# Kernel tuning notes

Measured on AMD Instinct MI355X. Metric: run time of the kernel, lower is better.

The kernel has to match this reference:

```python
import jax, jax.numpy as jnp
import numpy as np

TOPK = 2
ROUTED_SCALING_FACTOR = 1.0


def setup_inputs() -> dict:
    key = jax.random.key(0)
    k1, k2 = jax.random.split(key)
    N, D, E = 8192, 4096, 64
    x = jax.random.normal(k1, (N, D), dtype=jnp.float32)
    expert_embeddings = jax.random.normal(k2, (E, D), dtype=jnp.float32) * 0.02
    gate_bias = jnp.zeros((E,), dtype=jnp.float32)
    return {"x": x, "expert_embeddings": expert_embeddings, "gate_bias": gate_bias}


def reference(x, expert_embeddings, gate_bias):
    # logits: (N, E) = x @ W^T, computed in fp32 as in the original
    logits = jnp.einsum('nd,ed->ne', x.astype(jnp.float32), expert_embeddings.astype(jnp.float32))
    scores = jax.nn.sigmoid(logits)
    biased_scores = scores + gate_bias  # bias only affects expert selection
    _, indices = jax.lax.top_k(biased_scores, TOPK)  # (N, topk)
    weights = jnp.take_along_axis(scores, indices, axis=-1)  # gather unbiased scores
    weights = weights / jnp.sum(weights, axis=-1, keepdims=True)
    weights = weights * ROUTED_SCALING_FACTOR
    return weights, indices, scores
```

## Files before the change

### kernel.cpp

```cpp
#include <hip/hip_runtime.h>
#include <hip/hip_bf16.h>
#include <math.h>

#define NROWS 8192
#define DDIM  4096
#define NEXP  64
#define KSPLIT 16
#define KCHUNK (DDIM / KSPLIT)
#define KSTEPS (KCHUNK / 32)

typedef __attribute__((ext_vector_type(8))) short bf16x8;
typedef __attribute__((ext_vector_type(4))) float f32x4;

__device__ inline unsigned short bf16_rne(float f) {
    unsigned u = __builtin_bit_cast(unsigned, f);
    u += 0x7FFF + ((u >> 16) & 1);
    return (unsigned short)(u >> 16);
}

__device__ inline void split8(const float* xf, bf16x8& hi, bf16x8& lo) {
#pragma unroll
    for (int j = 0; j < 8; j++) {
        const unsigned short h = bf16_rne(xf[j]);
        const float hf = __builtin_bit_cast(float, (unsigned)h << 16);
        hi[j] = (short)h;
        lo[j] = (short)bf16_rne(xf[j] - hf);
    }
}

__global__ __launch_bounds__(256) void wfrag_kernel(
    const float* __restrict__ w, unsigned short* __restrict__ whi,
    unsigned short* __restrict__ wlo, float* __restrict__ logits)
{
    const int kc = blockIdx.x;
    const int t  = threadIdx.x >> 6;
    const int l  = threadIdx.x & 63;
    const int e  = t * 16 + (l & 15);
    const int k0 = kc * 32 + ((l >> 4) * 8);
    const float* p = w + (size_t)e * DDIM + k0;
    float xf[8];
    *(float4*)&xf[0] = *(const float4*)p;
    *(float4*)&xf[4] = *(const float4*)(p + 4);
    bf16x8 hi, lo;
    split8(xf, hi, lo);
    const size_t off = ((size_t)(kc * 4 + t) * 64 + l) * 8;
    *(bf16x8*)(whi + off) = hi;
    *(bf16x8*)(wlo + off) = lo;

    const float4 z = {0.f, 0.f, 0.f, 0.f};
    float4* lz = (float4*)logits;
    const int base = (blockIdx.x * 256 + threadIdx.x) * 4;
#pragma unroll
    for (int j = 0; j < 4; j++) lz[base + j] = z;
}

__global__ __launch_bounds__(256) void gemm_partial_kernel(
    const float* __restrict__ x, const unsigned short* __restrict__ whi,
    const unsigned short* __restrict__ wlo, float* __restrict__ logits)
{
    const int tid = threadIdx.x;
    const int wv  = tid >> 6;
    const int l   = tid & 63;
    const int q   = l >> 4;
    const int col = l & 15;
    const int r0  = blockIdx.x * 128 + wv * 32;
    const int kh  = blockIdx.y;
    const int kb  = kh * KCHUNK;

    const float* xp0 = x + (size_t)(r0 + col) * DDIM + kb + q * 8;
    const float* xp1 = xp0 + (size_t)16 * DDIM;
    const unsigned short* bhp = whi + ((size_t)(kb / 32) * 4 * 64 + l) * 8;
    const unsigned short* blp = wlo + ((size_t)(kb / 32) * 4 * 64 + l) * 8;

    f32x4 acc[2][4];
#pragma unroll
    for (int m = 0; m < 2; m++)
#pragma unroll
        for (int t = 0; t < 4; t++) acc[m][t] = f32x4{0, 0, 0, 0};

    float xf[2][2][8];
    *(float4*)&xf[0][0][0] = *(const float4*)(xp0);
    *(float4*)&xf[0][0][4] = *(const float4*)(xp0 + 4);
    *(float4*)&xf[0][1][0] = *(const float4*)(xp1);
    *(float4*)&xf[0][1][4] = *(const float4*)(xp1 + 4);

    for (int s = 0; s < KSTEPS; s++) {
        const int cur = s & 1, nxt = cur ^ 1;

        bf16x8 bh[4], bl[4];
        const unsigned short* bhs = bhp + (size_t)s * 4 * 64 * 8;
        const unsigned short* bls = blp + (size_t)s * 4 * 64 * 8;
#pragma unroll
        for (int t = 0; t < 4; t++) {
            bh[t] = *(const bf16x8*)(bhs + (size_t)t * 64 * 8);
            bl[t] = *(const bf16x8*)(bls + (size_t)t * 64 * 8);
        }

        if (s + 1 < KSTEPS) {
            const float* xn0 = xp0 + (s + 1) * 32;
            const float* xn1 = xp1 + (s + 1) * 32;
            *(float4*)&xf[nxt][0][0] = *(const float4*)(xn0);
            *(float4*)&xf[nxt][0][4] = *(const float4*)(xn0 + 4);
            *(float4*)&xf[nxt][1][0] = *(const float4*)(xn1);
            *(float4*)&xf[nxt][1][4] = *(const float4*)(xn1 + 4);
        }

        bf16x8 ah[2], al[2];
        split8(xf[cur][0], ah[0], al[0]);
        split8(xf[cur][1], ah[1], al[1]);
#pragma unroll
        for (int m = 0; m < 2; m++)
#pragma unroll
            for (int t = 0; t < 4; t++) {
                acc[m][t] = __builtin_amdgcn_mfma_f32_16x16x32_bf16(ah[m], bh[t], acc[m][t], 0, 0, 0);
                acc[m][t] = __builtin_amdgcn_mfma_f32_16x16x32_bf16(ah[m], bl[t], acc[m][t], 0, 0, 0);
                acc[m][t] = __builtin_amdgcn_mfma_f32_16x16x32_bf16(al[m], bh[t], acc[m][t], 0, 0, 0);
            }
    }

#pragma unroll
    for (int m = 0; m < 2; m++)
#pragma unroll
        for (int t = 0; t < 4; t++)
#pragma unroll
            for (int r = 0; r < 4; r++)
                unsafeAtomicAdd(
                    &logits[(size_t)(r0 + m * 16 + q * 4 + r) * NEXP + t * 16 + col],
                    acc[m][t][r]);
}

__global__ __launch_bounds__(256) void gate_topk_kernel(
    const float* __restrict__ logits, const float* __restrict__ bias,
    float* __restrict__ out)
{
    const int tid = threadIdx.x;
    const int e   = tid & 63;
    const int row = blockIdx.x * 4 + (tid >> 6);
    const size_t idx = (size_t)row * NEXP + e;

    const float logit = logits[idx];
    const float score = 1.0f / (1.0f + expf(-logit));
    out[(size_t)4 * NROWS + idx] = score;

    const float biased = score + bias[e];

    float v = biased; int bi = e;
#pragma unroll
    for (int off = 32; off; off >>= 1) {
        const float ov = __shfl_xor(v, off);
        const int   oi = __shfl_xor(bi, off);
        if (ov > v || (ov == v && oi < bi)) { v = ov; bi = oi; }
    }
    const int i1 = bi;

    float v2 = (e == i1) ? -INFINITY : biased;
    int bi2 = e;
#pragma unroll
    for (int off = 32; off; off >>= 1) {
        const float ov = __shfl_xor(v2, off);
        const int   oi = __shfl_xor(bi2, off);
        if (ov > v2 || (ov == v2 && oi < bi2)) { v2 = ov; bi2 = oi; }
    }
    const int i2 = bi2;

    const float s1 = __shfl(score, i1);
    const float s2 = __shfl(score, i2);
    if (e == 0) {
        const float inv = 1.0f / (s1 + s2);
        out[(size_t)row * 2 + 0] = s1 * inv;
        out[(size_t)row * 2 + 1] = s2 * inv;
        out[(size_t)2 * NROWS + row * 2 + 0] = (float)i1;
        out[(size_t)2 * NROWS + row * 2 + 1] = (float)i2;
    }
}

extern "C" void kernel_launch(void* const* d_in, const int* in_sizes, int n_in,
                              void* d_out, int out_size, void* d_ws, size_t ws_size,
                              hipStream_t stream)
{
    const float* x    = (const float*)d_in[0];
    const float* w    = (const float*)d_in[1];
    const float* bias = (const float*)d_in[2];
    float* out  = (float*)d_out;

    float* logits = (float*)d_ws;
    const size_t logits_bytes = (size_t)NROWS * NEXP * 4;
    unsigned short* whi = (unsigned short*)((char*)d_ws + logits_bytes);
    unsigned short* wlo = whi + (size_t)NEXP * DDIM;

    wfrag_kernel<<<DDIM / 32, 256, 0, stream>>>(w, whi, wlo, logits);
    dim3 g1(NROWS / 128, KSPLIT);
    gemm_partial_kernel<<<g1, 256, 0, stream>>>(x, whi, wlo, logits);
    gate_topk_kernel<<<NROWS / 4, 256, 0, stream>>>(logits, bias, out);
}
```

Baseline: 214.6 us.

## Fuse gate/top-k into split-K GEMM via last-block counter

Removes the separate gate_topk kernel. Each row-tile keeps an atomic counter, and the last of the KSPLIT blocks to finish runs the sigmoid, top-2 and normalization for its 128 rows. This saves one kernel launch and a global re-read pass over the logits, but the epilogue is serialized onto a few late blocks and the kernel gains extra fences and atomics.

```diff
diff --git a/kernel.cpp b/kernel.cpp
--- a/kernel.cpp
+++ b/kernel.cpp
@@ -30,7 +30,8 @@
 
 __global__ __launch_bounds__(256) void wfrag_kernel(
     const float* __restrict__ w, unsigned short* __restrict__ whi,
-    unsigned short* __restrict__ wlo, float* __restrict__ logits)
+    unsigned short* __restrict__ wlo, float* __restrict__ logits,
+    unsigned* __restrict__ cnt)
 {
     const int kc = blockIdx.x;
     const int t  = threadIdx.x >> 6;
@@ -52,12 +53,18 @@
     const int base = (blockIdx.x * 256 + threadIdx.x) * 4;
 #pragma unroll
     for (int j = 0; j < 4; j++) lz[base + j] = z;
-}
-
-__global__ __launch_bounds__(256) void gemm_partial_kernel(
+
+    if (blockIdx.x == 0 && threadIdx.x < 64) cnt[threadIdx.x] = 0;
+}
+
+__global__ __launch_bounds__(256) void gemm_gate_kernel(
     const float* __restrict__ x, const unsigned short* __restrict__ whi,
-    const unsigned short* __restrict__ wlo, float* __restrict__ logits)
+    const unsigned short* __restrict__ wlo, const float* __restrict__ bias,
+    float* __restrict__ logits, unsigned* __restrict__ cnt,
+    float* __restrict__ out)
 {
+    __shared__ bool last_flag;
+
     const int tid = threadIdx.x;
     const int wv  = tid >> 6;
     const int l   = tid & 63;
@@ -127,50 +134,63 @@
                 unsafeAtomicAdd(
                     &logits[(size_t)(r0 + m * 16 + q * 4 + r) * NEXP + t * 16 + col],
                     acc[m][t][r]);
-}
-
-__global__ __launch_bounds__(256) void gate_topk_kernel(
-    const float* __restrict__ logits, const float* __restrict__ bias,
-    float* __restrict__ out)
-{
-    const int tid = threadIdx.x;
-    const int e   = tid & 63;
-    const int row = blockIdx.x * 4 + (tid >> 6);
-    const size_t idx = (size_t)row * NEXP + e;
-
-    const float logit = logits[idx];
-    const float score = 1.0f / (1.0f + expf(-logit));
-    out[(size_t)4 * NROWS + idx] = score;
-
-    const float biased = score + bias[e];
-
-    float v = biased; int bi = e;
-#pragma unroll
-    for (int off = 32; off; off >>= 1) {
-        const float ov = __shfl_xor(v, off);
-        const int   oi = __shfl_xor(bi, off);
-        if (ov > v || (ov == v && oi < bi)) { v = ov; bi = oi; }
-    }
-    const int i1 = bi;
-
-    float v2 = (e == i1) ? -INFINITY : biased;
-    int bi2 = e;
-#pragma unroll
-    for (int off = 32; off; off >>= 1) {
-        const float ov = __shfl_xor(v2, off);
-        const int   oi = __shfl_xor(bi2, off);
-        if (ov > v2 || (ov == v2 && oi < bi2)) { v2 = ov; bi2 = oi; }
-    }
-    const int i2 = bi2;
-
-    const float s1 = __shfl(score, i1);
-    const float s2 = __shfl(score, i2);
-    if (e == 0) {
-        const float inv = 1.0f / (s1 + s2);
-        out[(size_t)row * 2 + 0] = s1 * inv;
-        out[(size_t)row * 2 + 1] = s2 * inv;
-        out[(size_t)2 * NROWS + row * 2 + 0] = (float)i1;
-        out[(size_t)2 * NROWS + row * 2 + 1] = (float)i2;
+
+    __syncthreads();
+    if (tid == 0) {
+        __threadfence();
+        const unsigned old = __hip_atomic_fetch_add(
+            &cnt[blockIdx.x], 1u, __ATOMIC_ACQ_REL, __HIP_MEMORY_SCOPE_AGENT);
+        last_flag = (old == KSPLIT - 1);
+    }
+    __syncthreads();
+    if (!last_flag) return;
+
+    const int rbase = blockIdx.x * 128;
+    const float be  = bias[l];
+    for (int c = 0; c < 4; c++) {
+        float lv[8];
+#pragma unroll
+        for (int j = 0; j < 8; j++)
+            lv[j] = __hip_atomic_load(
+                &logits[(size_t)(rbase + wv * 32 + c * 8 + j) * NEXP + l],
+                __ATOMIC_RELAXED, __HIP_MEMORY_SCOPE_AGENT);
+#pragma unroll
+        for (int j = 0; j < 8; j++) {
+            const int row = rbase + wv * 32 + c * 8 + j;
+            const float score = 1.0f / (1.0f + expf(-lv[j]));
+            out[(size_t)4 * NROWS + (size_t)row * NEXP + l] = score;
+
+            const float biased = score + be;
+
+            float v = biased; int bi = l;
+#pragma unroll
+            for (int off = 32; off; off >>= 1) {
+                const float ov = __shfl_xor(v, off);
+                const int   oi = __shfl_xor(bi, off);
+                if (ov > v || (ov == v && oi < bi)) { v = ov; bi = oi; }
+            }
+            const int i1 = bi;
+
+            float v2 = (l == i1) ? -INFINITY : biased;
+            int bi2 = l;
+#pragma unroll
+            for (int off = 32; off; off >>= 1) {
+                const float ov = __shfl_xor(v2, off);
+                const int   oi = __shfl_xor(bi2, off);
+                if (ov > v2 || (ov == v2 && oi < bi2)) { v2 = ov; bi2 = oi; }
+            }
+            const int i2 = bi2;
+
+            const float s1 = __shfl(score, i1);
+            const float s2 = __shfl(score, i2);
+            if (l == 0) {
+                const float inv = 1.0f / (s1 + s2);
+                out[(size_t)row * 2 + 0] = s1 * inv;
+                out[(size_t)row * 2 + 1] = s2 * inv;
+                out[(size_t)2 * NROWS + row * 2 + 0] = (float)i1;
+                out[(size_t)2 * NROWS + row * 2 + 1] = (float)i2;
+            }
+        }
     }
 }
 
@@ -187,9 +207,9 @@
     const size_t logits_bytes = (size_t)NROWS * NEXP * 4;
     unsigned short* whi = (unsigned short*)((char*)d_ws + logits_bytes);
     unsigned short* wlo = whi + (size_t)NEXP * DDIM;
-
-    wfrag_kernel<<<DDIM / 32, 256, 0, stream>>>(w, whi, wlo, logits);
+    unsigned* cnt = (unsigned*)(wlo + (size_t)NEXP * DDIM);
+
+    wfrag_kernel<<<DDIM / 32, 256, 0, stream>>>(w, whi, wlo, logits, cnt);
     dim3 g1(NROWS / 128, KSPLIT);
-    gemm_partial_kernel<<<g1, 256, 0, stream>>>(x, whi, wlo, logits);
-    gate_topk_kernel<<<NROWS / 4, 256, 0, stream>>>(logits, bias, out);
-}
+    gemm_gate_kernel<<<g1, 256, 0, stream>>>(x, whi, wlo, bias, logits, cnt, out);
+}
```

New measurement: 350.0 us. 1.63x slower.
